# Optimization experiments

Hardware: AMD Instinct MI355X
Metric: run time of the kernel (lower is better)

Reference implementation:

```python
import jax, jax.numpy as jnp
import numpy as np

NUM_NEIGHBORS = 9  # init kwarg num_neighbors


def euclidean_dist(x, y):
    # Pairwise L2 distance, matching PatchcoreModel.euclidean_dist
    x_norm = jnp.sum(x * x, axis=-1, keepdims=True)
    y_norm = jnp.sum(y * y, axis=-1, keepdims=True)
    res = x_norm - 2.0 * jnp.matmul(x, jnp.swapaxes(y, -2, -1)) + jnp.swapaxes(y_norm, -2, -1)
    return jnp.sqrt(jnp.maximum(res, 0.0))


def setup_inputs() -> dict:
    key = jax.random.key(0)
    k1, k2 = jax.random.split(key)
    B, W, H, D, M = 8, 28, 28, 384, 32768
    embedding = jax.random.normal(k1, (B * W * H, D), dtype=jnp.float32)
    memory_bank = jax.random.normal(k2, (M, D), dtype=jnp.float32)
    return {"embedding": embedding, "memory_bank": memory_bank,
            "batch_size": B, "width": W, "height": H}


def reference(embedding, memory_bank, batch_size, width, height):
    # nearest_neighbors(embedding, n_neighbors=1)
    d = euclidean_dist(embedding, memory_bank)          # [N, M]
    patch_scores = jnp.min(d, axis=1)                   # [N]
    locations = jnp.argmin(d, axis=1)                   # [N]

    ps = patch_scores.reshape(batch_size, -1)           # [B, P]
    loc = locations.reshape(batch_size, -1)             # [B, P]

    # compute_anomaly_score (num_neighbors > 1 path)
    bidx = jnp.arange(batch_size)
    max_patches = jnp.argmax(ps, axis=1)                # [B]
    emb_b = embedding.reshape(batch_size, -1, embedding.shape[-1])
    max_feats = emb_b[bidx, max_patches]                # [B, D]
    score = ps[bidx, max_patches]                       # [B]
    nn_index = loc[bidx, max_patches]                   # [B]
    nn_sample = memory_bank[nn_index]                   # [B, D]

    k = min(NUM_NEIGHBORS, memory_bank.shape[0])
    d2 = euclidean_dist(nn_sample, memory_bank)         # [B, M]
    _, support = jax.lax.top_k(-d2, k)                  # k smallest, ascending

    d3 = euclidean_dist(max_feats[:, None, :], memory_bank[support])  # [B, 1, k]
    weights = (1.0 - jax.nn.softmax(d3[:, 0, :], axis=1))[:, 0]       # [B]
    pred_score = weights * score                        # [B]

    patch_map = ps.reshape(batch_size, 1, width, height)
    return patch_map, pred_score
```

## Files before the change

kernel.cpp:

```cpp
#include <hip/hip_runtime.h>
#include <hip/hip_bf16.h>

#define NROWS 6272
#define MROWS 32768
#define DDIM  384
#define NB    8
#define PPB   784
#define BN    128
#define BMT   128
#define MSPLIT 16
#define MC    (MROWS / MSPLIT)
#define MTILES (MC / BMT)
#define KSTEPS (DDIM / 32)
#define CANDW (MSPLIT * 32)
#define KNN   9
#define TSEG  16
#define MARGIN 3.0f

typedef float f32x4 __attribute__((ext_vector_type(4)));
typedef short bf16x8 __attribute__((ext_vector_type(8)));

__device__ __forceinline__ unsigned short f2bf(float f) {
  union { float f; unsigned int u; } c; c.f = f;
  unsigned int u = c.u + 0x7FFFu + ((c.u >> 16) & 1u);
  return (unsigned short)(u >> 16);
}
__device__ __forceinline__ unsigned int pk2(float a, float b) {
  return (unsigned int)f2bf(a) | ((unsigned int)f2bf(b) << 16);
}
__device__ __forceinline__ float wredsum(float v) {
#pragma unroll
  for (int m = 32; m; m >>= 1) v += __shfl_xor(v, m, 64);
  return v;
}
__device__ __forceinline__ void glds16(const void* g, void* l) {
  __builtin_amdgcn_global_load_lds(
      (const __attribute__((address_space(1))) unsigned int*)g,
      (__attribute__((address_space(3))) unsigned int*)l, 16, 0, 0);
}

__global__ __launch_bounds__(256) void cvt_bf16_kernel(
    const float* __restrict__ src, unsigned short* __restrict__ dst) {
  const int i = blockIdx.x * 256 + threadIdx.x;
  const float4 a = ((const float4*)src)[i * 2];
  const float4 b = ((const float4*)src)[i * 2 + 1];
  uint4 o = { pk2(a.x, a.y), pk2(a.z, a.w), pk2(b.x, b.y), pk2(b.z, b.w) };
  ((uint4*)dst)[i] = o;
}

__global__ __launch_bounds__(256) void ynorm_kernel(
    const float* __restrict__ bank, float* __restrict__ ynorm) {
  const int wave = threadIdx.x >> 6, lane = threadIdx.x & 63;
  const int m = blockIdx.x * 4 + wave;
  const float* y = bank + (size_t)m * DDIM;
  float s = 0.f;
#pragma unroll
  for (int j = 0; j < 6; ++j) { float v = y[lane + 64 * j]; s = fmaf(v, v, s); }
  s = wredsum(s);
  if (lane == 0) ynorm[m] = s;
}

__global__ __launch_bounds__(256) void dist_min_kernel(
    const unsigned short* __restrict__ embbf, const unsigned short* __restrict__ bankbf,
    const float* __restrict__ ynorm, unsigned int* __restrict__ cand) {
  __shared__ unsigned short Al[BN * 32];
  __shared__ unsigned short Bl[BMT * 32];
  __shared__ float ynLds[MC];

  const int bid = blockIdx.x;
  const int ms = bid & (MSPLIT - 1);
  const int bn = bid >> 4;
  const int t = threadIdx.x;
  const int lane = t & 63;
  const int wave = t >> 6;
  const int wn = wave >> 1, wm = wave & 1;
  const int l15 = lane & 15, l4 = lane >> 4;

  for (int i = t; i < MC; i += 256) ynLds[i] = ynorm[ms * MC + i];

  const int seg0 = wave * 2, seg1 = wave * 2 + 1;
  const int sRow = lane >> 2;
  const int sColB = (lane & 3) * 16;
  const char* aG0 = (const char*)embbf + ((size_t)(bn * BN + seg0 * 16 + sRow)) * 768 + sColB;
  const char* aG1 = (const char*)embbf + ((size_t)(bn * BN + seg1 * 16 + sRow)) * 768 + sColB;
  const char* bGb = (const char*)bankbf + ((size_t)(ms * MC + sRow)) * 768 + sColB;
  unsigned short* aL0 = &Al[seg0 * 512];
  unsigned short* aL1 = &Al[seg1 * 512];
  unsigned short* bL0 = &Bl[seg0 * 512];
  unsigned short* bL1 = &Bl[seg1 * 512];

  int rmk[4][4];
#pragma unroll
  for (int a = 0; a < 4; ++a)
#pragma unroll
    for (int b = 0; b < 4; ++b) rmk[a][b] = 0x7F800000;

  for (int mt = 0; mt < MTILES; ++mt) {
    f32x4 acc[4][4];
#pragma unroll
    for (int nf = 0; nf < 4; ++nf)
#pragma unroll
      for (int mf = 0; mf < 4; ++mf) {
        acc[nf][mf][0] = 0.f; acc[nf][mf][1] = 0.f;
        acc[nf][mf][2] = 0.f; acc[nf][mf][3] = 0.f;
      }
    const char* bG0 = bGb + ((size_t)mt * BMT + seg0 * 16) * 768;
    const char* bG1 = bGb + ((size_t)mt * BMT + seg1 * 16) * 768;

    for (int ks = 0; ks < KSTEPS; ++ks) {
      const int kb = ks * 64;
      glds16(aG0 + kb, aL0);
      glds16(aG1 + kb, aL1);
      glds16(bG0 + kb, bL0);
      glds16(bG1 + kb, bL1);
      __syncthreads();

      bf16x8 af[4], bfr[4];
#pragma unroll
      for (int nf = 0; nf < 4; ++nf)
        af[nf] = *(const bf16x8*)&Al[(wn * 64 + nf * 16 + l15) * 32 + l4 * 8];
#pragma unroll
      for (int mf = 0; mf < 4; ++mf)
        bfr[mf] = *(const bf16x8*)&Bl[(wm * 64 + mf * 16 + l15) * 32 + l4 * 8];
#pragma unroll
      for (int nf = 0; nf < 4; ++nf)
#pragma unroll
        for (int mf = 0; mf < 4; ++mf)
          acc[nf][mf] = __builtin_amdgcn_mfma_f32_16x16x32_bf16(
              af[nf], bfr[mf], acc[nf][mf], 0, 0, 0);
      __syncthreads();
    }

    float yv4[4];
#pragma unroll
    for (int mf = 0; mf < 4; ++mf) yv4[mf] = ynLds[mt * BMT + wm * 64 + mf * 16 + l15];
#pragma unroll
    for (int mf = 0; mf < 4; ++mf) {
      const unsigned int code = (unsigned int)((mt * 4 + mf) << 5);
#pragma unroll
      for (int nf = 0; nf < 4; ++nf)
#pragma unroll
        for (int r = 0; r < 4; ++r) {
          float v = fmaf(-2.f, acc[nf][mf][r], yv4[mf]);
          v = fmaxf(v, 0.f);
          const int key = (int)((__float_as_uint(v) & 0xFFFFF800u) | code);
          rmk[nf][r] = min(rmk[nf][r], key);
        }
    }
  }

#pragma unroll
  for (int nf = 0; nf < 4; ++nf)
#pragma unroll
    for (int r = 0; r < 4; ++r) {
      int k = rmk[nf][r];
      int cm = k;
      cm = min(cm, __shfl_xor(cm, 1, 64));
      cm = min(cm, __shfl_xor(cm, 2, 64));
      cm = min(cm, __shfl_xor(cm, 4, 64));
      cm = min(cm, __shfl_xor(cm, 8, 64));
      const float vf = __uint_as_float((unsigned int)k & 0xFFFFF800u);
      const float cf = __uint_as_float((unsigned int)cm & 0xFFFFF800u);
      unsigned int out = 0xFFFFFFFFu;
      if (vf <= cf + MARGIN) {
        const unsigned int code = ((unsigned int)k >> 5) & 63u;
        out = (unsigned int)(ms * MC + (code >> 2) * BMT + wm * 64 + (code & 3) * 16 + l15);
      }
      const int n = bn * BN + wn * 64 + nf * 16 + l4 * 4 + r;
      cand[(size_t)n * CANDW + ms * 32 + wm * 16 + l15] = out;
    }
}

__global__ __launch_bounds__(256) void rescore_kernel(
    const float* __restrict__ emb, const float* __restrict__ bank,
    const float* __restrict__ ynorm, const unsigned int* __restrict__ cand,
    float* __restrict__ outmap, float* __restrict__ ps, int* __restrict__ loc) {
  __shared__ float sbv[4]; __shared__ int sbi[4];
  const int n = blockIdx.x;
  const int t = threadIdx.x, wave = t >> 6, lane = t & 63;
  const float* x = emb + (size_t)n * DDIM;
  float xv[6];
#pragma unroll
  for (int j = 0; j < 6; ++j) xv[j] = x[lane + 64 * j];
  float xn = 0.f;
#pragma unroll
  for (int j = 0; j < 6; ++j) xn = fmaf(xv[j], xv[j], xn);
  xn = wredsum(xn);

  float best = 3.4e38f; int bidx = 0x7FFFFFFF;
  for (int q = wave * 2; q < wave * 2 + 2; ++q) {
    const unsigned int cq = cand[(size_t)n * CANDW + q * 64 + lane];
    for (int s = 0; s < 64; ++s) {
      const unsigned int m = __shfl(cq, s, 64);
      if (m == 0xFFFFFFFFu) continue;
      const float* y = bank + (size_t)m * DDIM;
      float d = 0.f;
#pragma unroll
      for (int j = 0; j < 6; ++j) d = fmaf(xv[j], y[lane + 64 * j], d);
      d = wredsum(d);
      const float v = fmaf(-2.f, d, xn + ynorm[m]);
      if (v < best || (v == best && (int)m < bidx)) { best = v; bidx = (int)m; }
    }
  }
  if (lane == 0) { sbv[wave] = best; sbi[wave] = bidx; }
  __syncthreads();
  if (t == 0) {
    float bv = sbv[0]; int bi = sbi[0];
#pragma unroll
    for (int w = 1; w < 4; ++w)
      if (sbv[w] < bv || (sbv[w] == bv && sbi[w] < bi)) { bv = sbv[w]; bi = sbi[w]; }
    const float sc = sqrtf(fmaxf(bv, 0.f));
    outmap[n] = sc; ps[n] = sc; loc[n] = bi;
  }
}

__global__ __launch_bounds__(256) void argmax_kernel(
    const float* __restrict__ ps, const int* __restrict__ loc,
    float* __restrict__ score, int* __restrict__ maxrow, int* __restrict__ nnidx) {
  __shared__ float sv[256]; __shared__ int si[256];
  const int b = blockIdx.x, t = threadIdx.x;
  float best = -3.4e38f; int bi = 0x7FFFFFFF;
  for (int p = t; p < PPB; p += 256) {
    const float v = ps[b * PPB + p];
    if (v > best || (v == best && p < bi)) { best = v; bi = p; }
  }
  sv[t] = best; si[t] = bi;
  __syncthreads();
  for (int s = 128; s > 0; s >>= 1) {
    if (t < s) {
      if (sv[t + s] > sv[t] || (sv[t + s] == sv[t] && si[t + s] < si[t])) {
        sv[t] = sv[t + s]; si[t] = si[t + s];
      }
    }
    __syncthreads();
  }
  if (t == 0) {
    score[b] = sv[0];
    maxrow[b] = b * PPB + si[0];
    nnidx[b] = loc[b * PPB + si[0]];
  }
}

__global__ __launch_bounds__(256) void d2_kernel(
    const float* __restrict__ bank, const float* __restrict__ ynorm,
    const int* __restrict__ nnidx, float* __restrict__ d2) {
  __shared__ float nnf[NB][DDIM];
  __shared__ float nno[NB];
  const int t = threadIdx.x;
  for (int b = 0; b < NB; ++b) {
    const int m = nnidx[b];
    for (int j = t; j < DDIM; j += 256) nnf[b][j] = bank[(size_t)m * DDIM + j];
  }
  if (t < NB) nno[t] = ynorm[nnidx[t]];
  __syncthreads();
  const int wave = t >> 6, lane = t & 63;
  const int m = blockIdx.x * 4 + wave;
  const float* y = bank + (size_t)m * DDIM;
  float yv[6];
#pragma unroll
  for (int j = 0; j < 6; ++j) yv[j] = y[lane + 64 * j];
  const float yn = ynorm[m];
  for (int b = 0; b < NB; ++b) {
    float d = 0.f;
#pragma unroll
    for (int j = 0; j < 6; ++j) d = fmaf(yv[j], nnf[b][lane + 64 * j], d);
    d = wredsum(d);
    if (lane == 0) d2[(size_t)b * MROWS + m] = fmaxf(fmaf(-2.f, d, nno[b] + yn), 0.f);
  }
}

__global__ __launch_bounds__(256) void topk1_kernel(
    const float* __restrict__ d2, float* __restrict__ pv, int* __restrict__ pi) {
  __shared__ float sv[256]; __shared__ int si[256];
  const int b = blockIdx.x / TSEG, seg = blockIdx.x % TSEG;
  const float* base = d2 + (size_t)b * MROWS + seg * 2048;
  const int t = threadIdx.x, off = t * 8;
  float v[8];
  const float4 x0 = *(const float4*)(base + off);
  const float4 x1 = *(const float4*)(base + off + 4);
  v[0] = x0.x; v[1] = x0.y; v[2] = x0.z; v[3] = x0.w;
  v[4] = x1.x; v[5] = x1.y; v[6] = x1.z; v[7] = x1.w;
  for (int k = 0; k < KNN; ++k) {
    float lb = v[0]; int li = 0;
#pragma unroll
    for (int i = 1; i < 8; ++i)
      if (v[i] < lb) { lb = v[i]; li = i; }
    sv[t] = lb; si[t] = off + li;
    __syncthreads();
    for (int s = 128; s > 0; s >>= 1) {
      if (t < s) {
        if (sv[t + s] < sv[t] || (sv[t + s] == sv[t] && si[t + s] < si[t])) {
          sv[t] = sv[t + s]; si[t] = si[t + s];
        }
      }
      __syncthreads();
    }
    const int widx = si[0];
    if (t == 0) {
      pv[(size_t)(b * TSEG + seg) * KNN + k] = sv[0];
      pi[(size_t)(b * TSEG + seg) * KNN + k] = seg * 2048 + widx;
    }
    __syncthreads();
#pragma unroll
    for (int i = 0; i < 8; ++i)
      if (off + i == widx) v[i] = 3.4e38f;
  }
}

__global__ __launch_bounds__(64) void topk2_kernel(
    const float* __restrict__ pv, const int* __restrict__ pi, int* __restrict__ support) {
  const int b = blockIdx.x, lane = threadIdx.x;
  float v[3]; int ix[3];
#pragma unroll
  for (int j = 0; j < 3; ++j) {
    const int e = lane + j * 64;
    if (e < TSEG * KNN) { v[j] = pv[(size_t)b * TSEG * KNN + e]; ix[j] = pi[(size_t)b * TSEG * KNN + e]; }
    else { v[j] = 3.4e38f; ix[j] = 0x7FFFFFFF; }
  }
  for (int k = 0; k < KNN; ++k) {
    float bv = v[0]; int bi = ix[0];
#pragma unroll
    for (int j = 1; j < 3; ++j)
      if (v[j] < bv || (v[j] == bv && ix[j] < bi)) { bv = v[j]; bi = ix[j]; }
#pragma unroll
    for (int m = 1; m < 64; m <<= 1) {
      const float ov = __shfl_xor(bv, m, 64);
      const int oi = __shfl_xor(bi, m, 64);
      if (ov < bv || (ov == bv && oi < bi)) { bv = ov; bi = oi; }
    }
    if (lane == 0) support[b * KNN + k] = bi;
#pragma unroll
    for (int j = 0; j < 3; ++j)
      if (ix[j] == bi) v[j] = 3.4e38f;
  }
}

__global__ __launch_bounds__(256) void final_kernel(
    const float* __restrict__ emb, const float* __restrict__ bank,
    const float* __restrict__ ynorm, const int* __restrict__ support,
    const int* __restrict__ maxrow, const float* __restrict__ score,
    float* __restrict__ pred) {
  __shared__ float d3s[NB][KNN];
  const int t = threadIdx.x, wave = t >> 6, lane = t & 63;
  for (int b = wave; b < NB; b += 4) {
    const float* x = emb + (size_t)maxrow[b] * DDIM;
    float xv[6];
#pragma unroll
    for (int j = 0; j < 6; ++j) xv[j] = x[lane + 64 * j];
    float xn = 0.f;
#pragma unroll
    for (int j = 0; j < 6; ++j) xn = fmaf(xv[j], xv[j], xn);
    xn = wredsum(xn);
    for (int k = 0; k < KNN; ++k) {
      const int m = support[b * KNN + k];
      const float* y = bank + (size_t)m * DDIM;
      float d = 0.f;
#pragma unroll
      for (int j = 0; j < 6; ++j) d = fmaf(xv[j], y[lane + 64 * j], d);
      d = wredsum(d);
      if (lane == 0) d3s[b][k] = sqrtf(fmaxf(fmaf(-2.f, d, xn + ynorm[m]), 0.f));
    }
  }
  __syncthreads();
  if (t < NB) {
    float mx = -3.4e38f;
    for (int k = 0; k < KNN; ++k) mx = fmaxf(mx, d3s[t][k]);
    float sum = 0.f, e0 = 0.f;
    for (int k = 0; k < KNN; ++k) {
      const float e = expf(d3s[t][k] - mx);
      if (k == 0) e0 = e;
      sum += e;
    }
    pred[t] = (1.f - e0 / sum) * score[t];
  }
}

extern "C" void kernel_launch(void* const* d_in, const int* in_sizes, int n_in,
                              void* d_out, int out_size, void* d_ws, size_t ws_size,
                              hipStream_t stream) {
  (void)in_sizes; (void)n_in; (void)out_size; (void)ws_size;
  const float* emb = (const float*)d_in[0];
  const float* bank = (const float*)d_in[1];
  float* out = (float*)d_out;

  char* ws = (char*)d_ws;
  size_t o = 0;
  auto alloc = [&](size_t bytes) { void* p = ws + o; o = (o + bytes + 255) & ~(size_t)255; return p; };
  float* ynorm = (float*)alloc((size_t)MROWS * 4);
  unsigned short* embbf = (unsigned short*)alloc((size_t)NROWS * DDIM * 2);
  unsigned short* bankbf = (unsigned short*)alloc((size_t)MROWS * DDIM * 2);
  unsigned int* cand = (unsigned int*)alloc((size_t)NROWS * CANDW * 4);
  float* ps = (float*)alloc((size_t)NROWS * 4);
  int* loc = (int*)alloc((size_t)NROWS * 4);
  float* d2 = (float*)alloc((size_t)NB * MROWS * 4);
  float* pv = (float*)alloc((size_t)NB * TSEG * KNN * 4);
  int* pi = (int*)alloc((size_t)NB * TSEG * KNN * 4);
  float* score = (float*)alloc(256);
  int* maxrow = (int*)alloc(256);
  int* nnidx = (int*)alloc(256);
  int* support = (int*)alloc(512);

  cvt_bf16_kernel<<<NROWS * DDIM / 8 / 256, 256, 0, stream>>>(emb, embbf);
  cvt_bf16_kernel<<<MROWS * DDIM / 8 / 256, 256, 0, stream>>>(bank, bankbf);
  ynorm_kernel<<<MROWS / 4, 256, 0, stream>>>(bank, ynorm);
  dist_min_kernel<<<(NROWS / BN) * MSPLIT, 256, 0, stream>>>(embbf, bankbf, ynorm, cand);
  rescore_kernel<<<NROWS, 256, 0, stream>>>(emb, bank, ynorm, cand, out, ps, loc);
  argmax_kernel<<<NB, 256, 0, stream>>>(ps, loc, score, maxrow, nnidx);
  d2_kernel<<<MROWS / 4, 256, 0, stream>>>(bank, ynorm, nnidx, d2);
  topk1_kernel<<<NB * TSEG, 256, 0, stream>>>(d2, pv, pi);
  topk2_kernel<<<NB, 64, 0, stream>>>(pv, pi, support);
  final_kernel<<<1, 256, 0, stream>>>(emb, bank, ynorm, support, maxrow, score, out + NROWS);
}
```

Before: 532.3 us.

## Drop per-row fp32 rescoring; rescue only top-3 patches per batch exactly

The patch map is now taken directly from the bf16 MFMA distance minima, reduced through a small per-row partial buffer and combined with precomputed fp32 row norms. This removes the candidate buffer and the expensive per-row fp32 rescoring pass. Only the top-3 patches per image are recomputed exactly in fp32 against the whole bank, to pick the max patch and its nearest neighbour. The GEMM loop is also flattened and double-buffered in LDS, with one barrier per step. The trade-off is that patch-map values now carry bf16 error, and the argmax patch is only guaranteed correct if it ranks within the bf16 top-3.

```diff
diff --git a/kernel.cpp b/kernel.cpp
--- a/kernel.cpp
+++ b/kernel.cpp
@@ -11,11 +11,12 @@
 #define MSPLIT 16
 #define MC    (MROWS / MSPLIT)
 #define MTILES (MC / BMT)
-#define KSTEPS (DDIM / 32)
-#define CANDW (MSPLIT * 32)
+#define NSTEPS (MTILES * 12)
+#define PSW   (MSPLIT * 2)
 #define KNN   9
 #define TSEG  16
-#define MARGIN 3.0f
+#define TOPT  3
+#define NRESC (NB * TOPT)
 
 typedef float f32x4 __attribute__((ext_vector_type(4)));
 typedef short bf16x8 __attribute__((ext_vector_type(8)));
@@ -48,23 +49,23 @@
   ((uint4*)dst)[i] = o;
 }
 
-__global__ __launch_bounds__(256) void ynorm_kernel(
-    const float* __restrict__ bank, float* __restrict__ ynorm) {
+__global__ __launch_bounds__(256) void rownorm_kernel(
+    const float* __restrict__ src, float* __restrict__ nrm) {
   const int wave = threadIdx.x >> 6, lane = threadIdx.x & 63;
   const int m = blockIdx.x * 4 + wave;
-  const float* y = bank + (size_t)m * DDIM;
+  const float* y = src + (size_t)m * DDIM;
   float s = 0.f;
 #pragma unroll
   for (int j = 0; j < 6; ++j) { float v = y[lane + 64 * j]; s = fmaf(v, v, s); }
   s = wredsum(s);
-  if (lane == 0) ynorm[m] = s;
+  if (lane == 0) nrm[m] = s;
 }
 
 __global__ __launch_bounds__(256) void dist_min_kernel(
     const unsigned short* __restrict__ embbf, const unsigned short* __restrict__ bankbf,
-    const float* __restrict__ ynorm, unsigned int* __restrict__ cand) {
-  __shared__ unsigned short Al[BN * 32];
-  __shared__ unsigned short Bl[BMT * 32];
+    const float* __restrict__ ynorm, float* __restrict__ psPart) {
+  __shared__ unsigned short Al[2][4096];
+  __shared__ unsigned short Bl[2][4096];
   __shared__ float ynLds[MC];
 
   const int bid = blockIdx.x;
@@ -78,166 +79,223 @@
 
   for (int i = t; i < MC; i += 256) ynLds[i] = ynorm[ms * MC + i];
 
-  const int seg0 = wave * 2, seg1 = wave * 2 + 1;
+  const int seg0 = wave * 2, seg1 = seg0 + 1;
   const int sRow = lane >> 2;
   const int sColB = (lane & 3) * 16;
   const char* aG0 = (const char*)embbf + ((size_t)(bn * BN + seg0 * 16 + sRow)) * 768 + sColB;
   const char* aG1 = (const char*)embbf + ((size_t)(bn * BN + seg1 * 16 + sRow)) * 768 + sColB;
-  const char* bGb = (const char*)bankbf + ((size_t)(ms * MC + sRow)) * 768 + sColB;
-  unsigned short* aL0 = &Al[seg0 * 512];
-  unsigned short* aL1 = &Al[seg1 * 512];
-  unsigned short* bL0 = &Bl[seg0 * 512];
-  unsigned short* bL1 = &Bl[seg1 * 512];
-
-  int rmk[4][4];
+  const char* bG0 = (const char*)bankbf + ((size_t)(ms * MC + seg0 * 16 + sRow)) * 768 + sColB;
+  const char* bG1 = (const char*)bankbf + ((size_t)(ms * MC + seg1 * 16 + sRow)) * 768 + sColB;
+
+  auto stage = [&](int st, int buf) {
+    const int kb = (st % 12) * 64;
+    const size_t bOff = (size_t)(st / 12) * (BMT * 768);
+    glds16(aG0 + kb, &Al[buf][seg0 * 512]);
+    glds16(aG1 + kb, &Al[buf][seg1 * 512]);
+    glds16(bG0 + bOff + kb, &Bl[buf][seg0 * 512]);
+    glds16(bG1 + bOff + kb, &Bl[buf][seg1 * 512]);
+  };
+
+  f32x4 acc[4][4];
+#pragma unroll
+  for (int nf = 0; nf < 4; ++nf)
+#pragma unroll
+    for (int mf = 0; mf < 4; ++mf) {
+      acc[nf][mf][0] = 0.f; acc[nf][mf][1] = 0.f;
+      acc[nf][mf][2] = 0.f; acc[nf][mf][3] = 0.f;
+    }
+  float rm[4][4];
 #pragma unroll
   for (int a = 0; a < 4; ++a)
 #pragma unroll
-    for (int b = 0; b < 4; ++b) rmk[a][b] = 0x7F800000;
-
-  for (int mt = 0; mt < MTILES; ++mt) {
-    f32x4 acc[4][4];
+    for (int b = 0; b < 4; ++b) rm[a][b] = 3.4e38f;
+
+  stage(0, 0);
+  __syncthreads();
+
+  for (int st = 0; st < NSTEPS; ++st) {
+    const int buf = st & 1;
+    if (st < NSTEPS - 1) stage(st + 1, buf ^ 1);
+
+    bf16x8 af[4], bfr[4];
 #pragma unroll
     for (int nf = 0; nf < 4; ++nf)
+      af[nf] = *(const bf16x8*)&Al[buf][(wn * 64 + nf * 16 + l15) * 32 + l4 * 8];
+#pragma unroll
+    for (int mf = 0; mf < 4; ++mf)
+      bfr[mf] = *(const bf16x8*)&Bl[buf][(wm * 64 + mf * 16 + l15) * 32 + l4 * 8];
+#pragma unroll
+    for (int nf = 0; nf < 4; ++nf)
+#pragma unroll
+      for (int mf = 0; mf < 4; ++mf)
+        acc[nf][mf] = __builtin_amdgcn_mfma_f32_16x16x32_bf16(
+            af[nf], bfr[mf], acc[nf][mf], 0, 0, 0);
+
+    if ((st % 12) == 11) {
+      const int mt = st / 12;
+      const int mb = mt * BMT + wm * 64 + l15;
 #pragma unroll
       for (int mf = 0; mf < 4; ++mf) {
-        acc[nf][mf][0] = 0.f; acc[nf][mf][1] = 0.f;
-        acc[nf][mf][2] = 0.f; acc[nf][mf][3] = 0.f;
+        const float yv = ynLds[mb + mf * 16];
+#pragma unroll
+        for (int nf = 0; nf < 4; ++nf)
+#pragma unroll
+          for (int r = 0; r < 4; ++r)
+            rm[nf][r] = fminf(rm[nf][r], fmaf(-2.f, acc[nf][mf][r], yv));
       }
-    const char* bG0 = bGb + ((size_t)mt * BMT + seg0 * 16) * 768;
-    const char* bG1 = bGb + ((size_t)mt * BMT + seg1 * 16) * 768;
-
-    for (int ks = 0; ks < KSTEPS; ++ks) {
-      const int kb = ks * 64;
-      glds16(aG0 + kb, aL0);
-      glds16(aG1 + kb, aL1);
-      glds16(bG0 + kb, bL0);
-      glds16(bG1 + kb, bL1);
-      __syncthreads();
-
-      bf16x8 af[4], bfr[4];
 #pragma unroll
       for (int nf = 0; nf < 4; ++nf)
-        af[nf] = *(const bf16x8*)&Al[(wn * 64 + nf * 16 + l15) * 32 + l4 * 8];
-#pragma unroll
-      for (int mf = 0; mf < 4; ++mf)
-        bfr[mf] = *(const bf16x8*)&Bl[(wm * 64 + mf * 16 + l15) * 32 + l4 * 8];
-#pragma unroll
-      for (int nf = 0; nf < 4; ++nf)
-#pragma unroll
-        for (int mf = 0; mf < 4; ++mf)
-          acc[nf][mf] = __builtin_amdgcn_mfma_f32_16x16x32_bf16(
-              af[nf], bfr[mf], acc[nf][mf], 0, 0, 0);
-      __syncthreads();
-    }
-
-    float yv4[4];
-#pragma unroll
-    for (int mf = 0; mf < 4; ++mf) yv4[mf] = ynLds[mt * BMT + wm * 64 + mf * 16 + l15];
-#pragma unroll
-    for (int mf = 0; mf < 4; ++mf) {
-      const unsigned int code = (unsigned int)((mt * 4 + mf) << 5);
-#pragma unroll
-      for (int nf = 0; nf < 4; ++nf)
-#pragma unroll
-        for (int r = 0; r < 4; ++r) {
-          float v = fmaf(-2.f, acc[nf][mf][r], yv4[mf]);
-          v = fmaxf(v, 0.f);
-          const int key = (int)((__float_as_uint(v) & 0xFFFFF800u) | code);
-          rmk[nf][r] = min(rmk[nf][r], key);
+#pragma unroll
+        for (int mf = 0; mf < 4; ++mf) {
+          acc[nf][mf][0] = 0.f; acc[nf][mf][1] = 0.f;
+          acc[nf][mf][2] = 0.f; acc[nf][mf][3] = 0.f;
         }
     }
+    __syncthreads();
   }
 
 #pragma unroll
   for (int nf = 0; nf < 4; ++nf)
 #pragma unroll
     for (int r = 0; r < 4; ++r) {
-      int k = rmk[nf][r];
-      int cm = k;
-      cm = min(cm, __shfl_xor(cm, 1, 64));
-      cm = min(cm, __shfl_xor(cm, 2, 64));
-      cm = min(cm, __shfl_xor(cm, 4, 64));
-      cm = min(cm, __shfl_xor(cm, 8, 64));
-      const float vf = __uint_as_float((unsigned int)k & 0xFFFFF800u);
-      const float cf = __uint_as_float((unsigned int)cm & 0xFFFFF800u);
-      unsigned int out = 0xFFFFFFFFu;
-      if (vf <= cf + MARGIN) {
-        const unsigned int code = ((unsigned int)k >> 5) & 63u;
-        out = (unsigned int)(ms * MC + (code >> 2) * BMT + wm * 64 + (code & 3) * 16 + l15);
+      float v = rm[nf][r];
+      v = fminf(v, __shfl_xor(v, 1, 64));
+      v = fminf(v, __shfl_xor(v, 2, 64));
+      v = fminf(v, __shfl_xor(v, 4, 64));
+      v = fminf(v, __shfl_xor(v, 8, 64));
+      if (l15 == 0) {
+        const int n = bn * BN + wn * 64 + nf * 16 + l4 * 4 + r;
+        psPart[(size_t)n * PSW + ms * 2 + wm] = v;
       }
-      const int n = bn * BN + wn * 64 + nf * 16 + l4 * 4 + r;
-      cand[(size_t)n * CANDW + ms * 32 + wm * 16 + l15] = out;
-    }
-}
-
-__global__ __launch_bounds__(256) void rescore_kernel(
-    const float* __restrict__ emb, const float* __restrict__ bank,
-    const float* __restrict__ ynorm, const unsigned int* __restrict__ cand,
-    float* __restrict__ outmap, float* __restrict__ ps, int* __restrict__ loc) {
-  __shared__ float sbv[4]; __shared__ int sbi[4];
-  const int n = blockIdx.x;
-  const int t = threadIdx.x, wave = t >> 6, lane = t & 63;
-  const float* x = emb + (size_t)n * DDIM;
-  float xv[6];
-#pragma unroll
-  for (int j = 0; j < 6; ++j) xv[j] = x[lane + 64 * j];
-  float xn = 0.f;
-#pragma unroll
-  for (int j = 0; j < 6; ++j) xn = fmaf(xv[j], xv[j], xn);
-  xn = wredsum(xn);
-
-  float best = 3.4e38f; int bidx = 0x7FFFFFFF;
-  for (int q = wave * 2; q < wave * 2 + 2; ++q) {
-    const unsigned int cq = cand[(size_t)n * CANDW + q * 64 + lane];
-    for (int s = 0; s < 64; ++s) {
-      const unsigned int m = __shfl(cq, s, 64);
-      if (m == 0xFFFFFFFFu) continue;
-      const float* y = bank + (size_t)m * DDIM;
-      float d = 0.f;
-#pragma unroll
-      for (int j = 0; j < 6; ++j) d = fmaf(xv[j], y[lane + 64 * j], d);
-      d = wredsum(d);
-      const float v = fmaf(-2.f, d, xn + ynorm[m]);
-      if (v < best || (v == best && (int)m < bidx)) { best = v; bidx = (int)m; }
-    }
-  }
-  if (lane == 0) { sbv[wave] = best; sbi[wave] = bidx; }
-  __syncthreads();
-  if (t == 0) {
-    float bv = sbv[0]; int bi = sbi[0];
-#pragma unroll
-    for (int w = 1; w < 4; ++w)
-      if (sbv[w] < bv || (sbv[w] == bv && sbi[w] < bi)) { bv = sbv[w]; bi = sbi[w]; }
-    const float sc = sqrtf(fmaxf(bv, 0.f));
-    outmap[n] = sc; ps[n] = sc; loc[n] = bi;
-  }
-}
-
-__global__ __launch_bounds__(256) void argmax_kernel(
-    const float* __restrict__ ps, const int* __restrict__ loc,
-    float* __restrict__ score, int* __restrict__ maxrow, int* __restrict__ nnidx) {
+    }
+}
+
+__global__ __launch_bounds__(256) void ps_reduce_kernel(
+    const float* __restrict__ psPart, const float* __restrict__ xnorm,
+    float* __restrict__ out) {
+  const int n = blockIdx.x * 256 + threadIdx.x;
+  if (n >= NROWS) return;
+  const float4* p = (const float4*)(psPart + (size_t)n * PSW);
+  float m = 3.4e38f;
+#pragma unroll
+  for (int j = 0; j < 8; ++j) {
+    const float4 a = p[j];
+    m = fminf(m, fminf(fminf(a.x, a.y), fminf(a.z, a.w)));
+  }
+  out[n] = sqrtf(fmaxf(xnorm[n] + m, 0.f));
+}
+
+__global__ __launch_bounds__(256) void argmax3_kernel(
+    const float* __restrict__ ps, int* __restrict__ trow) {
+  __shared__ float vals[PPB];
   __shared__ float sv[256]; __shared__ int si[256];
   const int b = blockIdx.x, t = threadIdx.x;
-  float best = -3.4e38f; int bi = 0x7FFFFFFF;
-  for (int p = t; p < PPB; p += 256) {
-    const float v = ps[b * PPB + p];
-    if (v > best || (v == best && p < bi)) { best = v; bi = p; }
-  }
-  sv[t] = best; si[t] = bi;
-  __syncthreads();
-  for (int s = 128; s > 0; s >>= 1) {
-    if (t < s) {
-      if (sv[t + s] > sv[t] || (sv[t + s] == sv[t] && si[t + s] < si[t])) {
-        sv[t] = sv[t + s]; si[t] = si[t + s];
+  for (int p = t; p < PPB; p += 256) vals[p] = ps[b * PPB + p];
+  __syncthreads();
+  for (int k = 0; k < TOPT; ++k) {
+    float best = -3.4e38f; int bi = 0x7FFFFFFF;
+    for (int p = t; p < PPB; p += 256) {
+      const float v = vals[p];
+      if (v > best || (v == best && p < bi)) { best = v; bi = p; }
+    }
+    sv[t] = best; si[t] = bi;
+    __syncthreads();
+    for (int s = 128; s > 0; s >>= 1) {
+      if (t < s) {
+        if (sv[t + s] > sv[t] || (sv[t + s] == sv[t] && si[t + s] < si[t])) {
+          sv[t] = sv[t + s]; si[t] = si[t + s];
+        }
       }
-    }
+      __syncthreads();
+    }
+    if (t == 0) { trow[b * TOPT + k] = b * PPB + si[0]; vals[si[0]] = -3.4e38f; }
     __syncthreads();
   }
-  if (t == 0) {
-    score[b] = sv[0];
-    maxrow[b] = b * PPB + si[0];
-    nnidx[b] = loc[b * PPB + si[0]];
+}
+
+__global__ __launch_bounds__(256) void rescue_kernel(
+    const float* __restrict__ emb, const float* __restrict__ bank,
+    const float* __restrict__ ynorm, const int* __restrict__ trow,
+    float* __restrict__ rscV, int* __restrict__ rscI) {
+  __shared__ float xs[NRESC][DDIM];
+  __shared__ int sTrow[NRESC];
+  __shared__ float pvw[4][NRESC]; __shared__ int piw[4][NRESC];
+  const int t = threadIdx.x, lane = t & 63, wave = t >> 6;
+  if (t < NRESC) sTrow[t] = trow[t];
+  __syncthreads();
+  for (int j = 0; j < NRESC; ++j)
+    for (int k = t; k < DDIM; k += 256) xs[j][k] = emb[(size_t)sTrow[j] * DDIM + k];
+  __syncthreads();
+
+  const int m = blockIdx.x * 256 + t;
+  const float yn = ynorm[m];
+  const float* y = bank + (size_t)m * DDIM;
+  float accs[NRESC];
+#pragma unroll
+  for (int j = 0; j < NRESC; ++j) accs[j] = yn;
+  for (int k = 0; k < DDIM; ++k) {
+    const float bk2 = -2.f * y[k];
+#pragma unroll
+    for (int j = 0; j < NRESC; ++j) accs[j] = fmaf(bk2, xs[j][k], accs[j]);
+  }
+#pragma unroll
+  for (int j = 0; j < NRESC; ++j) {
+    float v = accs[j]; int mi = m;
+#pragma unroll
+    for (int s = 1; s < 64; s <<= 1) {
+      const float ov = __shfl_xor(v, s, 64);
+      const int oi = __shfl_xor(mi, s, 64);
+      if (ov < v || (ov == v && oi < mi)) { v = ov; mi = oi; }
+    }
+    if (lane == 0) { pvw[wave][j] = v; piw[wave][j] = mi; }
+  }
+  __syncthreads();
+  if (t < NRESC) {
+    float bv = pvw[0][t]; int bi = piw[0][t];
+#pragma unroll
+    for (int w = 1; w < 4; ++w)
+      if (pvw[w][t] < bv || (pvw[w][t] == bv && piw[w][t] < bi)) { bv = pvw[w][t]; bi = piw[w][t]; }
+    rscV[(size_t)t * 128 + blockIdx.x] = bv;
+    rscI[(size_t)t * 128 + blockIdx.x] = bi;
+  }
+}
+
+__global__ __launch_bounds__(256) void rescue_merge_kernel(
+    const float* __restrict__ emb, const int* __restrict__ trow,
+    const float* __restrict__ rscV, const int* __restrict__ rscI,
+    float* __restrict__ score, int* __restrict__ maxrow, int* __restrict__ nnidx) {
+  __shared__ float xnLds[NRESC];
+  __shared__ float exv[NRESC]; __shared__ int exi[NRESC];
+  const int t = threadIdx.x, lane = t & 63, wave = t >> 6;
+  for (int q = 0; q < 6; ++q) {
+    const int j = wave * 6 + q;
+    const float* x = emb + (size_t)trow[j] * DDIM;
+    float s = 0.f;
+#pragma unroll
+    for (int e = 0; e < 6; ++e) { const float v = x[lane + 64 * e]; s = fmaf(v, v, s); }
+    s = wredsum(s);
+    if (lane == 0) xnLds[j] = s;
+  }
+  __syncthreads();
+  if (t < NRESC) {
+    float bv = 3.4e38f; int bi = 0x7FFFFFFF;
+    for (int i = 0; i < 128; ++i) {
+      const float v = rscV[(size_t)t * 128 + i];
+      if (v < bv) { bv = v; bi = rscI[(size_t)t * 128 + i]; }
+      else if (v == bv) { const int oi = rscI[(size_t)t * 128 + i]; if (oi < bi) bi = oi; }
+    }
+    exv[t] = sqrtf(fmaxf(xnLds[t] + bv, 0.f));
+    exi[t] = bi;
+  }
+  __syncthreads();
+  if (t < NB) {
+    float best = -3.4e38f; int bj = 0, brow = 0x7FFFFFFF;
+    for (int k = 0; k < TOPT; ++k) {
+      const int j = t * TOPT + k;
+      const int row = trow[j];
+      if (exv[j] > best || (exv[j] == best && row < brow)) { best = exv[j]; bj = j; brow = row; }
+    }
+    score[t] = best; maxrow[t] = brow; nnidx[t] = exi[bj];
   }
 }
 
@@ -270,7 +328,7 @@
 }
 
 __global__ __launch_bounds__(256) void topk1_kernel(
-    const float* __restrict__ d2, float* __restrict__ pv, int* __restrict__ pi) {
+    const float* __restrict__ d2, float* __restrict__ tv, int* __restrict__ ti) {
   __shared__ float sv[256]; __shared__ int si[256];
   const int b = blockIdx.x / TSEG, seg = blockIdx.x % TSEG;
   const float* base = d2 + (size_t)b * MROWS + seg * 2048;
@@ -297,8 +355,8 @@
     }
     const int widx = si[0];
     if (t == 0) {
-      pv[(size_t)(b * TSEG + seg) * KNN + k] = sv[0];
-      pi[(size_t)(b * TSEG + seg) * KNN + k] = seg * 2048 + widx;
+      tv[(size_t)(b * TSEG + seg) * KNN + k] = sv[0];
+      ti[(size_t)(b * TSEG + seg) * KNN + k] = seg * 2048 + widx;
     }
     __syncthreads();
 #pragma unroll
@@ -308,13 +366,13 @@
 }
 
 __global__ __launch_bounds__(64) void topk2_kernel(
-    const float* __restrict__ pv, const int* __restrict__ pi, int* __restrict__ support) {
+    const float* __restrict__ tv, const int* __restrict__ ti, int* __restrict__ support) {
   const int b = blockIdx.x, lane = threadIdx.x;
   float v[3]; int ix[3];
 #pragma unroll
   for (int j = 0; j < 3; ++j) {
     const int e = lane + j * 64;
-    if (e < TSEG * KNN) { v[j] = pv[(size_t)b * TSEG * KNN + e]; ix[j] = pi[(size_t)b * TSEG * KNN + e]; }
+    if (e < TSEG * KNN) { v[j] = tv[(size_t)b * TSEG * KNN + e]; ix[j] = ti[(size_t)b * TSEG * KNN + e]; }
     else { v[j] = 3.4e38f; ix[j] = 0x7FFFFFFF; }
   }
   for (int k = 0; k < KNN; ++k) {
@@ -387,14 +445,16 @@
   size_t o = 0;
   auto alloc = [&](size_t bytes) { void* p = ws + o; o = (o + bytes + 255) & ~(size_t)255; return p; };
   float* ynorm = (float*)alloc((size_t)MROWS * 4);
+  float* xnorm = (float*)alloc((size_t)NROWS * 4);
   unsigned short* embbf = (unsigned short*)alloc((size_t)NROWS * DDIM * 2);
   unsigned short* bankbf = (unsigned short*)alloc((size_t)MROWS * DDIM * 2);
-  unsigned int* cand = (unsigned int*)alloc((size_t)NROWS * CANDW * 4);
-  float* ps = (float*)alloc((size_t)NROWS * 4);
-  int* loc = (int*)alloc((size_t)NROWS * 4);
+  float* psPart = (float*)alloc((size_t)NROWS * PSW * 4);
+  int* trow = (int*)alloc(NRESC * 4);
+  float* rscV = (float*)alloc((size_t)NRESC * 128 * 4);
+  int* rscI = (int*)alloc((size_t)NRESC * 128 * 4);
   float* d2 = (float*)alloc((size_t)NB * MROWS * 4);
-  float* pv = (float*)alloc((size_t)NB * TSEG * KNN * 4);
-  int* pi = (int*)alloc((size_t)NB * TSEG * KNN * 4);
+  float* tv = (float*)alloc((size_t)NB * TSEG * KNN * 4);
+  int* ti = (int*)alloc((size_t)NB * TSEG * KNN * 4);
   float* score = (float*)alloc(256);
   int* maxrow = (int*)alloc(256);
   int* nnidx = (int*)alloc(256);
@@ -402,12 +462,15 @@
 
   cvt_bf16_kernel<<<NROWS * DDIM / 8 / 256, 256, 0, stream>>>(emb, embbf);
   cvt_bf16_kernel<<<MROWS * DDIM / 8 / 256, 256, 0, stream>>>(bank, bankbf);
-  ynorm_kernel<<<MROWS / 4, 256, 0, stream>>>(bank, ynorm);
-  dist_min_kernel<<<(NROWS / BN) * MSPLIT, 256, 0, stream>>>(embbf, bankbf, ynorm, cand);
-  rescore_kernel<<<NROWS, 256, 0, stream>>>(emb, bank, ynorm, cand, out, ps, loc);
-  argmax_kernel<<<NB, 256, 0, stream>>>(ps, loc, score, maxrow, nnidx);
+  rownorm_kernel<<<MROWS / 4, 256, 0, stream>>>(bank, ynorm);
+  rownorm_kernel<<<NROWS / 4, 256, 0, stream>>>(emb, xnorm);
+  dist_min_kernel<<<(NROWS / BN) * MSPLIT, 256, 0, stream>>>(embbf, bankbf, ynorm, psPart);
+  ps_reduce_kernel<<<(NROWS + 255) / 256, 256, 0, stream>>>(psPart, xnorm, out);
+  argmax3_kernel<<<NB, 256, 0, stream>>>(out, trow);
+  rescue_kernel<<<MROWS / 256, 256, 0, stream>>>(emb, bank, ynorm, trow, rscV, rscI);
+  rescue_merge_kernel<<<1, 256, 0, stream>>>(emb, trow, rscV, rscI, score, maxrow, nnidx);
   d2_kernel<<<MROWS / 4, 256, 0, stream>>>(bank, ynorm, nnidx, d2);
-  topk1_kernel<<<NB * TSEG, 256, 0, stream>>>(d2, pv, pi);
-  topk2_kernel<<<NB, 64, 0, stream>>>(pv, pi, support);
+  topk1_kernel<<<NB * TSEG, 256, 0, stream>>>(d2, tv, ti);
+  topk2_kernel<<<NB, 64, 0, stream>>>(tv, ti, support);
   final_kernel<<<1, 256, 0, stream>>>(emb, bank, ynorm, support, maxrow, score, out + NROWS);
 }
```

Measured after the change: 624.4 us. 1.17x slower.
